# Kernel optimization log

Measured on AMD Instinct MI355X. Metric: run time of the kernel, lower is better.

The kernel has to match this reference:

```python
import jax, jax.numpy as jnp
import numpy as np

F_TOT = 108
OUT_CH = 5
GNN_IN = 5


def setup_inputs() -> dict:
    key = jax.random.key(0)
    ks = jax.random.split(key, 24)
    B, S, N, E = 16, 1, 20000, 320000
    s = 0.1  # param init scale
    d = {}
    d["x"] = jax.random.normal(ks[0], (B, S, N, F_TOT), jnp.float32)
    d["edge_index"] = jax.random.randint(ks[1], (2, E), 0, N, dtype=jnp.int32)
    # four Conv1d(1, 5, k=24) branches
    for i, nm in enumerate(["t", "r", "tp", "ssr"]):
        d[f"w_{nm}"] = s * jax.random.normal(ks[2 + 2 * i], (OUT_CH, 1, 24), jnp.float32)
        d[f"b_{nm}"] = s * jax.random.normal(ks[3 + 2 * i], (OUT_CH,), jnp.float32)
    # fc1: 32 -> 20, fc2: 20 -> 5
    d["fc1_w"] = s * jax.random.normal(ks[10], (20, 12 + 4 * OUT_CH), jnp.float32)
    d["fc1_b"] = s * jax.random.normal(ks[11], (20,), jnp.float32)
    d["fc2_w"] = s * jax.random.normal(ks[12], (GNN_IN, 20), jnp.float32)
    d["fc2_b"] = s * jax.random.normal(ks[13], (GNN_IN,), jnp.float32)
    # SAGEConv(5 -> 20): lin_l (with bias, applied to mean-aggregated neighbors), lin_r (no bias, root)
    d["g1_wl"] = s * jax.random.normal(ks[14], (20, GNN_IN), jnp.float32)
    d["g1_bl"] = s * jax.random.normal(ks[15], (20,), jnp.float32)
    d["g1_wr"] = s * jax.random.normal(ks[16], (20, GNN_IN), jnp.float32)
    # SAGEConv(20 -> 1)
    d["g2_wl"] = s * jax.random.normal(ks[17], (1, 20), jnp.float32)
    d["g2_bl"] = s * jax.random.normal(ks[18], (1,), jnp.float32)
    d["g2_wr"] = s * jax.random.normal(ks[19], (1, 20), jnp.float32)
    return d


def _branch(xs, w, b):
    # Conv1d(in=1, out=5, k=24) over a length-24 window == a single dot product per channel.
    # xs: [NB, 24], w: [5, 1, 24] -> [NB, 5], then ReLU
    return jax.nn.relu(jnp.einsum('nk,ok->no', xs, w[:, 0, :]) + b)


def _sage(h, src, dst, wl, bl, wr, n_nodes):
    # PyG SAGEConv with mean aggregation: out = lin_l(mean_{j in N(i)} x_j) + lin_r(x_i)
    # h: [B, N, d]
    msg = jnp.transpose(h[:, src, :], (1, 0, 2))                    # [E, B, d]
    agg = jax.ops.segment_sum(msg, dst, num_segments=n_nodes)       # [N, B, d]
    deg = jax.ops.segment_sum(jnp.ones((src.shape[0],), h.dtype), dst, num_segments=n_nodes)
    mean = jnp.transpose(agg, (1, 0, 2)) / jnp.maximum(deg, 1.0)[None, :, None]  # [B, N, d]
    return mean @ wl.T + bl + h @ wr.T


def reference(x, edge_index, w_t, b_t, w_r, b_r, w_tp, b_tp, w_ssr, b_ssr,
              fc1_w, fc1_b, fc2_w, fc2_b, g1_wl, g1_bl, g1_wr, g2_wl, g2_bl, g2_wr):
    B, S, N, F = x.shape
    src, dst = edge_index[0], edge_index[1]
    # permute(2,0,1,3).reshape(N*B, S, F); S == 1
    xs = jnp.transpose(x, (2, 0, 1, 3)).reshape(N * B, S, F)[:, 0, :]  # [NB, 108]
    out_t = _branch(xs[:, 12:36], w_t, b_t)
    out_r = _branch(xs[:, 36:60], w_r, b_r)
    out_tp = _branch(xs[:, 60:84], w_tp, b_tp)
    out_ssr = _branch(xs[:, 84:108], w_ssr, b_ssr)
    feat = jnp.concatenate([xs[:, :12], out_t, out_r, out_tp, out_ssr], axis=1)  # [NB, 32]
    h = jax.nn.relu(feat @ fc1_w.T + fc1_b) @ fc2_w.T + fc2_b                    # [NB, 5]
    h = jnp.transpose(h.reshape(N, B, -1), (1, 0, 2))                            # [B, N, 5]
    h = _sage(h, src, dst, g1_wl, g1_bl, g1_wr, N)                               # [B, N, 20]
    h = _sage(h, src, dst, g2_wl, g2_bl, g2_wr, N)                               # [B, N, 1]
    return jnp.transpose(h, (0, 2, 1))                                           # [B, 1, N]
```

## Files before the change

kernel.cpp:

```cpp
#include <hip/hip_runtime.h>


__global__ void k_zero(int* __restrict__ cnt, int N) {
  int n = blockIdx.x * blockDim.x + threadIdx.x;
  if (n < N) cnt[n] = 0;
}

__global__ void k_count(const int* __restrict__ dst, int E, int* __restrict__ cnt) {
  int e = blockIdx.x * blockDim.x + threadIdx.x;
  if (e < E) atomicAdd(&cnt[dst[e]], 1);
}

__global__ __launch_bounds__(1024) void k_scan(const int* __restrict__ cnt, int N,
                                               int* __restrict__ row_ptr,
                                               int* __restrict__ cursor) {
  __shared__ int part[1024];
  int t = threadIdx.x;
  int chunk = (N + 1023) / 1024;
  int s0 = t * chunk, s1 = min(N, s0 + chunk);
  int sum = 0;
  for (int i = s0; i < s1; ++i) sum += cnt[i];
  part[t] = sum;
  __syncthreads();
  for (int off = 1; off < 1024; off <<= 1) {
    int v = (t >= off) ? part[t - off] : 0;
    __syncthreads();
    part[t] += v;
    __syncthreads();
  }
  int run = (t == 0) ? 0 : part[t - 1];
  for (int i = s0; i < s1; ++i) {
    row_ptr[i] = run; cursor[i] = run;
    run += cnt[i];
  }
  if (s1 == N) row_ptr[N] = run;
}

__global__ void k_scatter(const int* __restrict__ src, const int* __restrict__ dst, int E,
                          int* __restrict__ cursor, int* __restrict__ adj) {
  int e = blockIdx.x * blockDim.x + threadIdx.x;
  if (e < E) {
    int pos = atomicAdd(&cursor[dst[e]], 1);
    adj[pos] = src[e];
  }
}

__global__ __launch_bounds__(256) void k_mlp(
    const float* __restrict__ x,
    const float* __restrict__ w_t, const float* __restrict__ b_t,
    const float* __restrict__ w_r, const float* __restrict__ b_r,
    const float* __restrict__ w_tp, const float* __restrict__ b_tp,
    const float* __restrict__ w_ssr, const float* __restrict__ b_ssr,
    const float* __restrict__ f1w, const float* __restrict__ f1b,
    const float* __restrict__ f2w, const float* __restrict__ f2b,
    const float* __restrict__ g1_wl, const float* __restrict__ g1_wr,
    const float* __restrict__ g2_wl, const float* __restrict__ g2_wr,
    float2* __restrict__ F1v, float2* __restrict__ F2v, int N, int rows) {
  int rr = blockIdx.x * 256 + threadIdx.x;
  if (rr >= rows) return;

  const float4* xv = reinterpret_cast<const float4*>(x + (size_t)rr * 108);
  float4 v[27];
#pragma unroll
  for (int i = 0; i < 27; ++i) v[i] = xv[i];
#pragma unroll
  for (int i = 0; i < 27; ++i)
    asm volatile("" : "+v"(v[i].x), "+v"(v[i].y), "+v"(v[i].z), "+v"(v[i].w));
  __builtin_amdgcn_sched_barrier(0);

  float feat[32];
#pragma unroll
  for (int i = 0; i < 3; ++i) {
    feat[4 * i + 0] = v[i].x; feat[4 * i + 1] = v[i].y;
    feat[4 * i + 2] = v[i].z; feat[4 * i + 3] = v[i].w;
  }
  const float* cw[4] = {w_t, w_r, w_tp, w_ssr};
  const float* cb[4] = {b_t, b_r, b_tp, b_ssr};
#pragma unroll
  for (int br = 0; br < 4; ++br) {
    float acc[5];
#pragma unroll
    for (int o = 0; o < 5; ++o) acc[o] = cb[br][o];
#pragma unroll
    for (int q = 0; q < 6; ++q) {
      float4 w4 = v[3 + 6 * br + q];
#pragma unroll
      for (int o = 0; o < 5; ++o) {
        acc[o] = fmaf(w4.x, cw[br][o * 24 + 4 * q + 0], acc[o]);
        acc[o] = fmaf(w4.y, cw[br][o * 24 + 4 * q + 1], acc[o]);
        acc[o] = fmaf(w4.z, cw[br][o * 24 + 4 * q + 2], acc[o]);
        acc[o] = fmaf(w4.w, cw[br][o * 24 + 4 * q + 3], acc[o]);
      }
    }
#pragma unroll
    for (int o = 0; o < 5; ++o) feat[12 + br * 5 + o] = fmaxf(acc[o], 0.f);
  }

  float h20[20];
#pragma unroll
  for (int o = 0; o < 20; ++o) {
    float acc = f1b[o];
#pragma unroll
    for (int i = 0; i < 32; ++i) acc = fmaf(feat[i], f1w[o * 32 + i], acc);
    h20[o] = fmaxf(acc, 0.f);
  }
  float h5[5];
#pragma unroll
  for (int o = 0; o < 5; ++o) {
    float acc = f2b[o];
#pragma unroll
    for (int i = 0; i < 20; ++i) acc = fmaf(h20[i], f2w[o * 20 + i], acc);
    h5[o] = acc;
  }

  float sa = 0.f, sr1 = 0.f, sc = 0.f, sr2 = 0.f;
#pragma unroll
  for (int j = 0; j < 20; ++j) {
    float t1 = 0.f, t2 = 0.f;
#pragma unroll
    for (int k = 0; k < 5; ++k) {
      t1 = fmaf(g1_wl[j * 5 + k], h5[k], t1);
      t2 = fmaf(g1_wr[j * 5 + k], h5[k], t2);
    }
    float wl2 = g2_wl[j], wr2 = g2_wr[j];
    sa  = fmaf(wl2, t1, sa);
    sr1 = fmaf(wr2, t1, sr1);
    sc  = fmaf(wl2, t2, sc);
    sr2 = fmaf(wr2, t2, sr2);
  }

  int b = rr / N;
  int n = rr - b * N;
  F1v[n * 16 + b] = make_float2(sa, sr1);
  F2v[n * 16 + b] = make_float2(sc, sr2);
}

__global__ void k_agg1(const int* __restrict__ row_ptr, const int* __restrict__ adj,
                       const float2* __restrict__ F1v, const float2* __restrict__ F2v,
                       float* __restrict__ W, float* __restrict__ V, int N) {
  int t = blockIdx.x * blockDim.x + threadIdx.x;
  int g = t >> 4, b = t & 15;
  if (g >= N) return;
  int beg = row_ptr[g], end = row_ptr[g + 1];
  float sa = 0.f, sb = 0.f;
  for (int c = beg; c < end; c += 16) {
    int idx = c + b;
    int a = adj[idx < end ? idx : end - 1];
    int m = min(16, end - c);
#pragma unroll 4
    for (int k = 0; k < m; ++k) {
      int s = __shfl(a, k, 16);
      float2 f = F1v[s * 16 + b];
      sa += f.x; sb += f.y;
    }
  }
  float inv = 1.0f / fmaxf((float)(end - beg), 1.0f);
  float2 f2 = F2v[t];
  W[t] = sa * inv + f2.x;
  V[t] = sb * inv;
}

__global__ __launch_bounds__(256) void k_agg2(
    const int* __restrict__ row_ptr, const int* __restrict__ adj,
    const float* __restrict__ W, const float* __restrict__ V,
    const float2* __restrict__ F2v,
    const float* __restrict__ g1_bl, const float* __restrict__ g2_wl,
    const float* __restrict__ g2_wr, const float* __restrict__ g2_bl,
    float* __restrict__ out, int N) {
  __shared__ float tile[16][17];
  int t = blockIdx.x * 256 + threadIdx.x;
  int g = t >> 4, b = t & 15;
  float r = 0.f;
  if (g < N) {
    int beg = row_ptr[g], end = row_ptr[g + 1];
    float sw = 0.f;
    for (int c = beg; c < end; c += 16) {
      int idx = c + b;
      int a = adj[idx < end ? idx : end - 1];
      int m = min(16, end - c);
#pragma unroll 4
      for (int k = 0; k < m; ++k) {
        int s = __shfl(a, k, 16);
        sw += W[s * 16 + b];
      }
    }
    float kb1 = 0.f, kb2 = 0.f;
#pragma unroll
    for (int j = 0; j < 20; ++j) {
      kb1 = fmaf(g2_wl[j], g1_bl[j], kb1);
      kb2 = fmaf(g2_wr[j], g1_bl[j], kb2);
    }
    int deg = end - beg;
    float inv = 1.0f / fmaxf((float)deg, 1.0f);
    float chi = deg > 0 ? 1.f : 0.f;
    r = sw * inv + V[t] + F2v[t].y + kb1 * chi + kb2 + g2_bl[0];
  }
  int gl = (threadIdx.x >> 4);
  tile[b][gl] = r;
  __syncthreads();
  int b2 = threadIdx.x >> 4;
  int gl2 = threadIdx.x & 15;
  int n2 = blockIdx.x * 16 + gl2;
  if (n2 < N) out[(size_t)b2 * N + n2] = tile[b2][gl2];
}

extern "C" void kernel_launch(void* const* d_in, const int* in_sizes, int n_in,
                              void* d_out, int out_size, void* d_ws, size_t ws_size,
                              hipStream_t stream) {
  const float* x     = (const float*)d_in[0];
  const int*   ei    = (const int*)d_in[1];
  const float* w_t   = (const float*)d_in[2];
  const float* b_t   = (const float*)d_in[3];
  const float* w_r   = (const float*)d_in[4];
  const float* b_r   = (const float*)d_in[5];
  const float* w_tp  = (const float*)d_in[6];
  const float* b_tp  = (const float*)d_in[7];
  const float* w_ssr = (const float*)d_in[8];
  const float* b_ssr = (const float*)d_in[9];
  const float* f1w   = (const float*)d_in[10];
  const float* f1b   = (const float*)d_in[11];
  const float* f2w   = (const float*)d_in[12];
  const float* f2b   = (const float*)d_in[13];
  const float* g1_wl = (const float*)d_in[14];
  const float* g1_bl = (const float*)d_in[15];
  const float* g1_wr = (const float*)d_in[16];
  const float* g2_wl = (const float*)d_in[17];
  const float* g2_bl = (const float*)d_in[18];
  const float* g2_wr = (const float*)d_in[19];
  float* out = (float*)d_out;

  const int E = in_sizes[1] / 2;
  const int N = out_size / 16;
  const int rows = out_size;
  const int* src = ei;
  const int* dst = ei + E;

  float* ws  = (float*)d_ws;
  float2* F1v = (float2*)ws;
  float2* F2v = F1v + (size_t)16 * N;
  float*  W   = (float*)(F2v + (size_t)16 * N);
  float*  V   = W + (size_t)16 * N;
  int* cnt     = (int*)(V + (size_t)16 * N);
  int* row_ptr = cnt + N;
  int* cursor  = row_ptr + N + 1;
  int* adj     = cursor + N;

  int nb16 = (N * 16 + 255) / 256;

  k_zero<<<(N + 255) / 256, 256, 0, stream>>>(cnt, N);
  k_count<<<(E + 255) / 256, 256, 0, stream>>>(dst, E, cnt);
  k_scan<<<1, 1024, 0, stream>>>(cnt, N, row_ptr, cursor);
  k_scatter<<<(E + 255) / 256, 256, 0, stream>>>(src, dst, E, cursor, adj);
  k_mlp<<<(rows + 255) / 256, 256, 0, stream>>>(
      x, w_t, b_t, w_r, b_r, w_tp, b_tp, w_ssr, b_ssr,
      f1w, f1b, f2w, f2b, g1_wl, g1_wr, g2_wl, g2_wr, F1v, F2v, N, rows);
  k_agg1<<<nb16, 256, 0, stream>>>(row_ptr, adj, F1v, F2v, W, V, N);
  k_agg2<<<nb16, 256, 0, stream>>>(row_ptr, adj, W, V, F2v,
                                   g1_bl, g2_wl, g2_wr, g2_bl, out, N);
}
```

Measured before the change: 148.6 us.

## Fold fc2 and SAGE weights into precomputed coefficients; split MLP rows across four lanes

Precomputes in the scan kernel a 4x20 coefficient matrix, its bias terms and the bias constants. These fold fc2 together with both SAGE linear layers, so the per-row work after fc1 becomes four 20-length dot products. The MLP kernel now uses four threads per row, one conv branch each, and stages weights and intermediates in shared memory with padded strides. The goal is to cut per-thread register pressure from the 27 float4 loads and drop redundant FMAs, at the cost of several block barriers, shared-memory traffic and per-row loads split across lanes. It also removes the unroll pragmas on the aggregation loops.

```diff
diff --git a/kernel.cpp b/kernel.cpp
--- a/kernel.cpp
+++ b/kernel.cpp
@@ -1,5 +1,11 @@
 #include <hip/hip_runtime.h>
 
+
+#define F1W 500
+#define F1B 1160
+#define CO  1180
+#define FEAT 1266
+#define HL   3378
 
 __global__ void k_zero(int* __restrict__ cnt, int N) {
   int n = blockIdx.x * blockDim.x + threadIdx.x;
@@ -11,11 +17,62 @@
   if (e < E) atomicAdd(&cnt[dst[e]], 1);
 }
 
-__global__ __launch_bounds__(1024) void k_scan(const int* __restrict__ cnt, int N,
-                                               int* __restrict__ row_ptr,
-                                               int* __restrict__ cursor) {
+__global__ __launch_bounds__(1024) void k_scan(
+    const int* __restrict__ cnt, int N,
+    int* __restrict__ row_ptr, int* __restrict__ cursor,
+    const float* __restrict__ f2w, const float* __restrict__ f2b,
+    const float* __restrict__ g1_wl, const float* __restrict__ g1_bl,
+    const float* __restrict__ g1_wr, const float* __restrict__ g2_wl,
+    const float* __restrict__ g2_wr, float* __restrict__ coef) {
+  int t = threadIdx.x;
+
+  if (t < 21) {
+    float a[5], r1[5], c[5], r2[5];
+#pragma unroll
+    for (int k = 0; k < 5; ++k) { a[k] = 0.f; r1[k] = 0.f; c[k] = 0.f; r2[k] = 0.f; }
+#pragma unroll
+    for (int j = 0; j < 20; ++j) {
+      float wl2 = g2_wl[j], wr2 = g2_wr[j];
+#pragma unroll
+      for (int k = 0; k < 5; ++k) {
+        float wl1 = g1_wl[j * 5 + k], wr1 = g1_wr[j * 5 + k];
+        a[k]  = fmaf(wl2, wl1, a[k]);
+        r1[k] = fmaf(wr2, wl1, r1[k]);
+        c[k]  = fmaf(wl2, wr1, c[k]);
+        r2[k] = fmaf(wr2, wr1, r2[k]);
+      }
+    }
+    if (t < 20) {
+      float A = 0.f, R1 = 0.f, C = 0.f, R2 = 0.f;
+#pragma unroll
+      for (int k = 0; k < 5; ++k) {
+        float w = f2w[k * 20 + t];
+        A  = fmaf(a[k],  w, A);
+        R1 = fmaf(r1[k], w, R1);
+        C  = fmaf(c[k],  w, C);
+        R2 = fmaf(r2[k], w, R2);
+      }
+      coef[t] = A; coef[20 + t] = R1; coef[40 + t] = C; coef[60 + t] = R2;
+    } else {
+      float ca = 0.f, cr1 = 0.f, cc = 0.f, cr2 = 0.f;
+#pragma unroll
+      for (int k = 0; k < 5; ++k) {
+        float b = f2b[k];
+        ca = fmaf(a[k], b, ca);  cr1 = fmaf(r1[k], b, cr1);
+        cc = fmaf(c[k], b, cc);  cr2 = fmaf(r2[k], b, cr2);
+      }
+      coef[80] = ca; coef[81] = cr1; coef[82] = cc; coef[83] = cr2;
+      float kb1 = 0.f, kb2 = 0.f;
+#pragma unroll
+      for (int j = 0; j < 20; ++j) {
+        kb1 = fmaf(g2_wl[j], g1_bl[j], kb1);
+        kb2 = fmaf(g2_wr[j], g1_bl[j], kb2);
+      }
+      coef[84] = kb1; coef[85] = kb2;
+    }
+  }
+
   __shared__ int part[1024];
-  int t = threadIdx.x;
   int chunk = (N + 1023) / 1024;
   int s0 = t * chunk, s1 = min(N, s0 + chunk);
   int sum = 0;
@@ -52,87 +109,88 @@
     const float* __restrict__ w_tp, const float* __restrict__ b_tp,
     const float* __restrict__ w_ssr, const float* __restrict__ b_ssr,
     const float* __restrict__ f1w, const float* __restrict__ f1b,
-    const float* __restrict__ f2w, const float* __restrict__ f2b,
-    const float* __restrict__ g1_wl, const float* __restrict__ g1_wr,
-    const float* __restrict__ g2_wl, const float* __restrict__ g2_wr,
+    const float* __restrict__ coef,
     float2* __restrict__ F1v, float2* __restrict__ F2v, int N, int rows) {
-  int rr = blockIdx.x * 256 + threadIdx.x;
-  if (rr >= rows) return;
+  __shared__ float S[4978];
+  const int t = threadIdx.x;
+  const int q = t & 3, r = t >> 2;
+  int rr = blockIdx.x * 64 + r;
+  bool live = rr < rows;
+  if (!live) rr = rows - 1;
 
   const float4* xv = reinterpret_cast<const float4*>(x + (size_t)rr * 108);
-  float4 v[27];
-#pragma unroll
-  for (int i = 0; i < 27; ++i) v[i] = xv[i];
-#pragma unroll
-  for (int i = 0; i < 27; ++i)
-    asm volatile("" : "+v"(v[i].x), "+v"(v[i].y), "+v"(v[i].z), "+v"(v[i].w));
-  __builtin_amdgcn_sched_barrier(0);
-
-  float feat[32];
-#pragma unroll
-  for (int i = 0; i < 3; ++i) {
-    feat[4 * i + 0] = v[i].x; feat[4 * i + 1] = v[i].y;
-    feat[4 * i + 2] = v[i].z; feat[4 * i + 3] = v[i].w;
-  }
-  const float* cw[4] = {w_t, w_r, w_tp, w_ssr};
-  const float* cb[4] = {b_t, b_r, b_tp, b_ssr};
-#pragma unroll
-  for (int br = 0; br < 4; ++br) {
-    float acc[5];
-#pragma unroll
-    for (int o = 0; o < 5; ++o) acc[o] = cb[br][o];
-#pragma unroll
-    for (int q = 0; q < 6; ++q) {
-      float4 w4 = v[3 + 6 * br + q];
-#pragma unroll
-      for (int o = 0; o < 5; ++o) {
-        acc[o] = fmaf(w4.x, cw[br][o * 24 + 4 * q + 0], acc[o]);
-        acc[o] = fmaf(w4.y, cw[br][o * 24 + 4 * q + 1], acc[o]);
-        acc[o] = fmaf(w4.z, cw[br][o * 24 + 4 * q + 2], acc[o]);
-        acc[o] = fmaf(w4.w, cw[br][o * 24 + 4 * q + 3], acc[o]);
-      }
-    }
-#pragma unroll
-    for (int o = 0; o < 5; ++o) feat[12 + br * 5 + o] = fmaxf(acc[o], 0.f);
-  }
-
-  float h20[20];
-#pragma unroll
-  for (int o = 0; o < 20; ++o) {
-    float acc = f1b[o];
-#pragma unroll
-    for (int i = 0; i < 32; ++i) acc = fmaf(feat[i], f1w[o * 32 + i], acc);
-    h20[o] = fmaxf(acc, 0.f);
-  }
-  float h5[5];
-#pragma unroll
-  for (int o = 0; o < 5; ++o) {
-    float acc = f2b[o];
-#pragma unroll
-    for (int i = 0; i < 20; ++i) acc = fmaf(h20[i], f2w[o * 20 + i], acc);
-    h5[o] = acc;
-  }
-
-  float sa = 0.f, sr1 = 0.f, sc = 0.f, sr2 = 0.f;
-#pragma unroll
-  for (int j = 0; j < 20; ++j) {
-    float t1 = 0.f, t2 = 0.f;
-#pragma unroll
-    for (int k = 0; k < 5; ++k) {
-      t1 = fmaf(g1_wl[j * 5 + k], h5[k], t1);
-      t2 = fmaf(g1_wr[j * 5 + k], h5[k], t2);
-    }
-    float wl2 = g2_wl[j], wr2 = g2_wr[j];
-    sa  = fmaf(wl2, t1, sa);
-    sr1 = fmaf(wr2, t1, sr1);
-    sc  = fmaf(wl2, t2, sc);
-    sr2 = fmaf(wr2, t2, sr2);
-  }
-
-  int b = rr / N;
-  int n = rr - b * N;
-  F1v[n * 16 + b] = make_float2(sa, sr1);
-  F2v[n * 16 + b] = make_float2(sc, sr2);
+  float4 bv[6];
+#pragma unroll
+  for (int i = 0; i < 6; ++i) bv[i] = xv[3 + 6 * q + i];
+  float4 pv = make_float4(0.f, 0.f, 0.f, 0.f);
+  if (q > 0) pv = xv[q - 1];
+
+  if (t < 120) {
+    S[t] = w_t[t]; S[120 + t] = w_r[t]; S[240 + t] = w_tp[t]; S[360 + t] = w_ssr[t];
+  }
+  if (t < 5) {
+    S[480 + t] = b_t[t]; S[485 + t] = b_r[t];
+    S[490 + t] = b_tp[t]; S[495 + t] = b_ssr[t];
+  }
+  for (int i = t; i < 640; i += 256) {
+    int o = i >> 5, k = i & 31;
+    S[F1W + o * 33 + k] = f1w[i];
+  }
+  if (t < 20) S[F1B + t] = f1b[t];
+  if (t >= 128 && t < 128 + 86) S[CO + t - 128] = coef[t - 128];
+  __syncthreads();
+
+  float acc[5];
+#pragma unroll
+  for (int o = 0; o < 5; ++o) acc[o] = S[480 + q * 5 + o];
+#pragma unroll
+  for (int i = 0; i < 6; ++i) {
+    float4 w4 = bv[i];
+#pragma unroll
+    for (int o = 0; o < 5; ++o) {
+      const int wb = q * 120 + o * 24 + 4 * i;
+      acc[o] = fmaf(w4.x, S[wb + 0], acc[o]);
+      acc[o] = fmaf(w4.y, S[wb + 1], acc[o]);
+      acc[o] = fmaf(w4.z, S[wb + 2], acc[o]);
+      acc[o] = fmaf(w4.w, S[wb + 3], acc[o]);
+    }
+  }
+  float* fr = &S[FEAT + r * 33];
+  if (q > 0) {
+    fr[4 * (q - 1) + 0] = pv.x; fr[4 * (q - 1) + 1] = pv.y;
+    fr[4 * (q - 1) + 2] = pv.z; fr[4 * (q - 1) + 3] = pv.w;
+  }
+#pragma unroll
+  for (int o = 0; o < 5; ++o) fr[12 + q * 5 + o] = fmaxf(acc[o], 0.f);
+  __syncthreads();
+
+  float a2[5];
+#pragma unroll
+  for (int j = 0; j < 5; ++j) a2[j] = S[F1B + q * 5 + j];
+#pragma unroll
+  for (int i = 0; i < 32; ++i) {
+    float f = fr[i];
+#pragma unroll
+    for (int j = 0; j < 5; ++j)
+      a2[j] = fmaf(f, S[F1W + (q * 5 + j) * 33 + i], a2[j]);
+  }
+  float* hr = &S[HL + r * 25];
+#pragma unroll
+  for (int j = 0; j < 5; ++j) hr[q * 5 + j] = fmaxf(a2[j], 0.f);
+  __syncthreads();
+
+  float s = S[CO + 80 + q];
+#pragma unroll
+  for (int i = 0; i < 20; ++i) s = fmaf(hr[i], S[CO + q * 20 + i], s);
+  hr[20 + q] = s;
+  __syncthreads();
+
+  if (q == 0 && live) {
+    int b = rr / N;
+    int n = rr - b * N;
+    F1v[n * 16 + b] = make_float2(hr[20], hr[21]);
+    F2v[n * 16 + b] = make_float2(hr[22], hr[23]);
+  }
 }
 
 __global__ void k_agg1(const int* __restrict__ row_ptr, const int* __restrict__ adj,
@@ -147,7 +205,6 @@
     int idx = c + b;
     int a = adj[idx < end ? idx : end - 1];
     int m = min(16, end - c);
-#pragma unroll 4
     for (int k = 0; k < m; ++k) {
       int s = __shfl(a, k, 16);
       float2 f = F1v[s * 16 + b];
@@ -163,10 +220,8 @@
 __global__ __launch_bounds__(256) void k_agg2(
     const int* __restrict__ row_ptr, const int* __restrict__ adj,
     const float* __restrict__ W, const float* __restrict__ V,
-    const float2* __restrict__ F2v,
-    const float* __restrict__ g1_bl, const float* __restrict__ g2_wl,
-    const float* __restrict__ g2_wr, const float* __restrict__ g2_bl,
-    float* __restrict__ out, int N) {
+    const float2* __restrict__ F2v, const float* __restrict__ coef,
+    const float* __restrict__ g2_bl, float* __restrict__ out, int N) {
   __shared__ float tile[16][17];
   int t = blockIdx.x * 256 + threadIdx.x;
   int g = t >> 4, b = t & 15;
@@ -178,22 +233,15 @@
       int idx = c + b;
       int a = adj[idx < end ? idx : end - 1];
       int m = min(16, end - c);
-#pragma unroll 4
       for (int k = 0; k < m; ++k) {
         int s = __shfl(a, k, 16);
         sw += W[s * 16 + b];
       }
     }
-    float kb1 = 0.f, kb2 = 0.f;
-#pragma unroll
-    for (int j = 0; j < 20; ++j) {
-      kb1 = fmaf(g2_wl[j], g1_bl[j], kb1);
-      kb2 = fmaf(g2_wr[j], g1_bl[j], kb2);
-    }
     int deg = end - beg;
     float inv = 1.0f / fmaxf((float)deg, 1.0f);
     float chi = deg > 0 ? 1.f : 0.f;
-    r = sw * inv + V[t] + F2v[t].y + kb1 * chi + kb2 + g2_bl[0];
+    r = sw * inv + V[t] + F2v[t].y + coef[84] * chi + coef[85] + g2_bl[0];
   }
   int gl = (threadIdx.x >> 4);
   tile[b][gl] = r;
@@ -240,7 +288,8 @@
   float2* F2v = F1v + (size_t)16 * N;
   float*  W   = (float*)(F2v + (size_t)16 * N);
   float*  V   = W + (size_t)16 * N;
-  int* cnt     = (int*)(V + (size_t)16 * N);
+  float*  coef = V + (size_t)16 * N;
+  int* cnt     = (int*)(coef + 128);
   int* row_ptr = cnt + N;
   int* cursor  = row_ptr + N + 1;
   int* adj     = cursor + N;
@@ -249,12 +298,12 @@
 
   k_zero<<<(N + 255) / 256, 256, 0, stream>>>(cnt, N);
   k_count<<<(E + 255) / 256, 256, 0, stream>>>(dst, E, cnt);
-  k_scan<<<1, 1024, 0, stream>>>(cnt, N, row_ptr, cursor);
+  k_scan<<<1, 1024, 0, stream>>>(cnt, N, row_ptr, cursor,
+                                 f2w, f2b, g1_wl, g1_bl, g1_wr, g2_wl, g2_wr, coef);
   k_scatter<<<(E + 255) / 256, 256, 0, stream>>>(src, dst, E, cursor, adj);
-  k_mlp<<<(rows + 255) / 256, 256, 0, stream>>>(
+  k_mlp<<<(rows + 63) / 64, 256, 0, stream>>>(
       x, w_t, b_t, w_r, b_r, w_tp, b_tp, w_ssr, b_ssr,
-      f1w, f1b, f2w, f2b, g1_wl, g1_wr, g2_wl, g2_wr, F1v, F2v, N, rows);
+      f1w, f1b, coef, F1v, F2v, N, rows);
   k_agg1<<<nb16, 256, 0, stream>>>(row_ptr, adj, F1v, F2v, W, V, N);
-  k_agg2<<<nb16, 256, 0, stream>>>(row_ptr, adj, W, V, F2v,
-                                   g1_bl, g2_wl, g2_wr, g2_bl, out, N);
-}
+  k_agg2<<<nb16, 256, 0, stream>>>(row_ptr, adj, W, V, F2v, coef, g2_bl, out, N);
+}
```

After: 145.5 us. 1.02x faster.
